# Kernel optimization log

Hardware: AMD Instinct MI355X
Metric: run time of the kernel (lower is better)

## Reference

```python
import jax, jax.numpy as jnp
import numpy as np
from jax import lax

NX, NY = 6, 6
NB = NX * NY            # 36 blocks
B, S = 64, 256          # batch, sample_count
EPS = 1e-6

def build_edges(nx, ny):
    edges = []
    for i in range(nx):
        for j in range(ny):
            for dx, dy in [(-1, 0), (0, -1), (0, 1), (1, 0)]:
                x, y = i + dx, j + dy
                if 0 <= x < nx and 0 <= y < ny:
                    edges.append((j * nx + i, y * nx + x))
    return np.array(edges, np.int32)   # (120, 2)

EDGES_NP = build_edges(NX, NY)
NE = len(EDGES_NP)  # 120

def setup_inputs() -> dict:
    key = jax.random.key(0)
    ks = jax.random.split(key, 24)
    f32 = jnp.float32
    d = {
        "image":      jax.random.normal(ks[0], (B, 1, 32, 32), f32),
        "edge_noise": jax.random.uniform(ks[1], (B, S, NE), f32),
        "u_s":        jax.random.uniform(ks[2], (B, S, NB), f32),
        "u_d":        jax.random.uniform(ks[3], (B, S, NB), f32),
        # CNN params (OIHW)
        "cw1": jax.random.normal(ks[4], (32, 1, 5, 5), f32) * 0.05,
        "cb1": jnp.zeros((32,), f32),
        "cw2": jax.random.normal(ks[5], (32, 32, 5, 5), f32) * 0.05,
        "cb2": jnp.zeros((32,), f32),
        "cw3": jax.random.normal(ks[6], (64, 32, 5, 5), f32) * 0.05,
        "cb3": jnp.zeros((64,), f32),
        "cw4": jax.random.normal(ks[7], (64, 64, 5, 5), f32) * 0.05,
        "cb4": jnp.zeros((64,), f32),
        # is_connected MLP
        "wc1": jax.random.normal(ks[8], (256, 256), f32) * 0.05,
        "bc1": jnp.zeros((256,), f32),
        "wc2": jax.random.normal(ks[9], (256, NE), f32) * 0.05,
        "bc2": jnp.zeros((NE,), f32),
        # is_endpoint MLP
        "we1": jax.random.normal(ks[10], (256, 256), f32) * 0.05,
        "be1": jnp.zeros((256,), f32),
        "we2": jax.random.normal(ks[11], (256, NB), f32) * 0.05,
        "be2": jnp.zeros((NB,), f32),
        "edges": jnp.asarray(EDGES_NP),  # (NE, 2) int32, constants
    }
    return d

def _conv(x, w, b):
    y = lax.conv_general_dilated(x, w, (1, 1), 'VALID',
                                 dimension_numbers=('NCHW', 'OIHW', 'NCHW'))
    return y + b[None, :, None, None]

def _pool2(x):
    return lax.reduce_window(x, -jnp.inf, lax.max, (1, 1, 2, 2), (1, 1, 2, 2), 'VALID')

def reference(image, edge_noise, u_s, u_d,
              cw1, cb1, cw2, cb2, cw3, cb3, cw4, cb4,
              wc1, bc1, wc2, bc2, we1, be1, we2, be2, edges):
    # ---- CNN feature extractor ----
    h = _conv(image, cw1, cb1)
    h = _conv(h, cw2, cb2)
    h = _pool2(h)
    h = _conv(h, cw3, cb3)
    h = _conv(h, cw4, cb4)
    h = _pool2(h)
    emb = h.reshape(h.shape[0], -1)              # (B, 256)

    # ---- heads ----
    p_conn = jax.nn.sigmoid(jax.nn.relu(emb @ wc1 + bc1) @ wc2 + bc2)   # (B, NE)
    p_ep   = jax.nn.sigmoid(jax.nn.relu(emb @ we1 + be1) @ we2 + be2)   # (B, NB)

    pc = jnp.clip(p_conn, EPS, 1.0 - EPS)
    pe = jnp.clip(p_ep, EPS, 1.0 - EPS)
    cat = pe / pe.sum(-1, keepdims=True)
    logcat = jnp.log(cat)                        # (B, NB)

    # ---- Monte-Carlo sampling (ISED blackbox) ----
    conn = (edge_noise < pc[:, None, :]).astype(pc.dtype)               # (B,S,NE) Bernoulli
    g_s = -jnp.log(-jnp.log(jnp.clip(u_s, EPS, 1.0 - EPS)))
    g_d = -jnp.log(-jnp.log(jnp.clip(u_d, EPS, 1.0 - EPS)))
    s_idx = jnp.argmax(logcat[:, None, :] + g_s, axis=-1)               # (B,S) categorical
    d_idx = jnp.argmax(logcat[:, None, :] + g_d, axis=-1)               # (B,S)

    # ---- batched BFS reachability via boolean matrix squaring ----
    oh_u = jax.nn.one_hot(edges[:, 0], NB, dtype=pc.dtype)              # (NE, NB)
    oh_v = jax.nn.one_hot(edges[:, 1], NB, dtype=pc.dtype)
    e_sym = jnp.einsum('eu,ev->euv', oh_u, oh_v) + jnp.einsum('eu,ev->evu', oh_u, oh_v)
    A = jnp.minimum(jnp.einsum('bse,euv->bsuv', conn, e_sym), 1.0)      # (B,S,36,36)

    R = jnp.minimum(A + jnp.eye(NB, dtype=A.dtype), 1.0)
    for _ in range(6):                           # (I+A)^(2^6), covers path len<=36
        R = jnp.minimum(R @ R, 1.0)
    P = jnp.minimum(A @ R, 1.0)                  # paths of length >= 1 (BFS semantics)

    Pv = jnp.take_along_axis(P, s_idx[:, :, None, None], axis=2)[:, :, 0, :]  # (B,S,36)
    exists = (jnp.take_along_axis(Pv, d_idx[:, :, None], axis=2)[:, :, 0] > 0.5).astype(pc.dtype)  # (B,S)

    # ---- sample-probability weighting (differentiable ISED estimator) ----
    logw = (conn * jnp.log(pc)[:, None, :] + (1.0 - conn) * jnp.log1p(-pc)[:, None, :]).sum(-1)
    logw = logw + jnp.take_along_axis(logcat, s_idx, axis=1) \
                + jnp.take_along_axis(logcat, d_idx, axis=1)            # (B,S)
    w = jax.nn.softmax(logw, axis=1)
    p1 = (w * exists).sum(axis=1)                # P(path exists)
    return jnp.stack([1.0 - p1, p1], axis=-1)    # (B, 2)
```

## Files before the change

### kernel.cpp

```cpp
#include <hip/hip_runtime.h>

typedef unsigned long long u64;
#define EPSF 1e-6f

__global__ __launch_bounds__(256) void k_conv1(const float* __restrict__ img,
                                               const float* __restrict__ cw1,
                                               const float* __restrict__ cb1,
                                               float* __restrict__ c1) {
  int slab = blockIdx.x, b = blockIdx.y;
  __shared__ float simg[32 * 33];
  for (int k = threadIdx.x; k < 1024; k += 256) {
    int y = k >> 5, x = k & 31;
    simg[y * 33 + x] = img[b * 1024 + k];
  }
  int ocl = threadIdx.x >> 5;
  int x = threadIdx.x & 31;
  int oc = slab * 8 + ocl;
  float w[25];
#pragma unroll
  for (int k = 0; k < 25; ++k) w[k] = cw1[oc * 25 + k];
  float bias = cb1[oc];
  __syncthreads();
  if (x < 28) {
    float acc[5];
#pragma unroll
    for (int k = 0; k < 5; ++k) acc[k] = bias;
    float* outp = c1 + (b * 32 + oc) * 784 + x;
#pragma unroll
    for (int r = 0; r < 32; ++r) {
      float in[5];
#pragma unroll
      for (int c = 0; c < 5; ++c) in[c] = simg[r * 33 + x + c];
#pragma unroll
      for (int ky = 0; ky < 5; ++ky) {
        int y = r - ky;
        if (y < 0 || y > 27) continue;
#pragma unroll
        for (int kx = 0; kx < 5; ++kx)
          acc[y % 5] = fmaf(w[ky * 5 + kx], in[kx], acc[y % 5]);
      }
      if (r >= 4) {
        int y = r - 4;
        outp[y * 28] = acc[y % 5];
        acc[y % 5] = bias;
      }
    }
  }
}

__global__ __launch_bounds__(192) void k_conv2(const float* __restrict__ c1,
                                               const float* __restrict__ cw2,
                                               const float* __restrict__ cb2,
                                               float* __restrict__ p1w) {
  int ocq = blockIdx.x, b = blockIdx.y;
  __shared__ float smem[18432];
  float* w2s = smem;
  float* sl = smem + 6400;
  int t = threadIdx.x;
  int g = t / 48, r48 = t % 48;
  int ocg = r48 / 24, row = r48 % 24;
  {
    const float4* src = (const float4*)(cw2 + ocq * 8 * 800);
    for (int k4 = t; k4 < 1600; k4 += 192) {
      float4 v = src[k4];
      float vv[4] = {v.x, v.y, v.z, v.w};
      int k = k4 * 4;
#pragma unroll
      for (int r = 0; r < 4; ++r) {
        int kk = k + r;
        int o = kk / 800, rest = kk % 800;
        w2s[rest * 8 + o] = vv[r];
      }
    }
  }
  float acc[4][24];
#pragma unroll
  for (int j = 0; j < 4; ++j)
#pragma unroll
    for (int c = 0; c < 24; ++c) acc[j][c] = 0.f;

  for (int icl = 0; icl < 8; ++icl) {
    int ic = g * 8 + icl;
    __syncthreads();
    {
      const float4* src = (const float4*)(c1 + (b * 32 + ic) * 784);
      float4* dst = (float4*)(sl + g * 784);
      for (int k = r48; k < 196; k += 48) dst[k] = src[k];
    }
    __syncthreads();
#pragma unroll
    for (int ky = 0; ky < 5; ++ky) {
      const float4* rp = (const float4*)(sl + g * 784 + (row + ky) * 28);
      float win[28];
#pragma unroll
      for (int q = 0; q < 7; ++q) {
        float4 v = rp[q];
        win[4 * q] = v.x; win[4 * q + 1] = v.y; win[4 * q + 2] = v.z; win[4 * q + 3] = v.w;
      }
      const float* wb = w2s + (ic * 25 + ky * 5) * 8 + ocg * 4;
#pragma unroll
      for (int kx = 0; kx < 5; ++kx) {
        float wq[4];
        *(float4*)wq = *(const float4*)(wb + kx * 8);
#pragma unroll
        for (int c = 0; c < 24; ++c) {
#pragma unroll
          for (int j = 0; j < 4; ++j) acc[j][c] = fmaf(wq[j], win[c + kx], acc[j][c]);
        }
      }
    }
  }
  __syncthreads();
  float* myred = smem + ((g * 2 + ocg) * 24 + row) * 96;
#pragma unroll
  for (int j = 0; j < 4; ++j)
#pragma unroll
    for (int c = 0; c < 24; ++c) myred[j * 24 + c] = acc[j][c];
  __syncthreads();
  if (g == 0) {
#pragma unroll
    for (int gg = 1; gg < 4; ++gg) {
      const float* rr = smem + ((gg * 2 + ocg) * 24 + row) * 96;
#pragma unroll
      for (int j = 0; j < 4; ++j)
#pragma unroll
        for (int c = 0; c < 24; ++c) acc[j][c] += rr[j * 24 + c];
    }
#pragma unroll
    for (int j = 0; j < 4; ++j) {
      float bias = cb2[ocq * 8 + ocg * 4 + j];
#pragma unroll
      for (int c = 0; c < 24; ++c) myred[j * 24 + c] = acc[j][c] + bias;
    }
  }
  __syncthreads();
  for (int k = t; k < 1152; k += 192) {
    int o = k / 144, rr2 = k % 144;
    int py = rr2 / 12, px = rr2 % 12;
    int og = o >> 2, j = o & 3;
    const float* b0 = smem + (og * 24 + 2 * py) * 96 + j * 24 + 2 * px;
    float m = fmaxf(fmaxf(b0[0], b0[1]), fmaxf(b0[96], b0[97]));
    p1w[(b * 32 + ocq * 8 + o) * 144 + py * 12 + px] = m;
  }
}

__global__ __launch_bounds__(256) void k_conv3(const float* __restrict__ p1w,
                                               const float* __restrict__ cw3,
                                               const float* __restrict__ cb3,
                                               float* __restrict__ c3) {
  int ocq = blockIdx.x, b = blockIdx.y;
  __shared__ float smem[17408];
  float* w3s = smem;
  float* ins = smem + 12800;
  int t = threadIdx.x;
  {
    const float4* src = (const float4*)(p1w + b * 32 * 144);
    float4* dst = (float4*)ins;
    for (int k = t; k < 1152; k += 256) dst[k] = src[k];
  }
  {
    const float4* src = (const float4*)(cw3 + ocq * 16 * 800);
    for (int k4 = t; k4 < 3200; k4 += 256) {
      float4 v = src[k4];
      float vv[4] = {v.x, v.y, v.z, v.w};
      int k = k4 * 4;
#pragma unroll
      for (int r = 0; r < 4; ++r) {
        int kk = k + r;
        int o = kk / 800, rest = kk % 800;
        w3s[rest * 16 + o] = vv[r];
      }
    }
  }
  int g = t >> 5, r32 = t & 31;
  int ocg = r32 >> 3, row = r32 & 7;
  float acc[4][8];
#pragma unroll
  for (int j = 0; j < 4; ++j)
#pragma unroll
    for (int c = 0; c < 8; ++c) acc[j][c] = 0.f;
  __syncthreads();
#pragma unroll
  for (int icl = 0; icl < 4; ++icl) {
    int ic = g * 4 + icl;
#pragma unroll
    for (int ky = 0; ky < 5; ++ky) {
      const float4* rp = (const float4*)(ins + ic * 144 + (row + ky) * 12);
      float win[12];
#pragma unroll
      for (int q = 0; q < 3; ++q) {
        float4 v = rp[q];
        win[4 * q] = v.x; win[4 * q + 1] = v.y; win[4 * q + 2] = v.z; win[4 * q + 3] = v.w;
      }
      const float* wb = w3s + (ic * 25 + ky * 5) * 16 + ocg * 4;
#pragma unroll
      for (int kx = 0; kx < 5; ++kx) {
        float wq[4];
        *(float4*)wq = *(const float4*)(wb + kx * 16);
#pragma unroll
        for (int c = 0; c < 8; ++c) {
#pragma unroll
          for (int j = 0; j < 4; ++j) acc[j][c] = fmaf(wq[j], win[c + kx], acc[j][c]);
        }
      }
    }
  }
  __syncthreads();
  float* myred = smem + t * 32;
#pragma unroll
  for (int j = 0; j < 4; ++j)
#pragma unroll
    for (int c = 0; c < 8; ++c) myred[j * 8 + c] = acc[j][c];
  __syncthreads();
  if (g == 0) {
#pragma unroll
    for (int gg = 1; gg < 8; ++gg) {
      const float* rr = smem + (gg * 32 + r32) * 32;
#pragma unroll
      for (int j = 0; j < 4; ++j)
#pragma unroll
        for (int c = 0; c < 8; ++c) acc[j][c] += rr[j * 8 + c];
    }
#pragma unroll
    for (int j = 0; j < 4; ++j) {
      float bias = cb3[ocq * 16 + ocg * 4 + j];
#pragma unroll
      for (int c = 0; c < 8; ++c)
        c3[(b * 64 + ocq * 16 + ocg * 4 + j) * 64 + row * 8 + c] = acc[j][c] + bias;
    }
  }
}

__global__ __launch_bounds__(256) void k_conv4(const float* __restrict__ c3,
                                               const float* __restrict__ cw4,
                                               const float* __restrict__ cb4,
                                               float* __restrict__ emb) {
  int ocq = blockIdx.x, b = blockIdx.y;
  __shared__ float smem[29696];
  float* w4s = smem;
  float* ins = smem + 25600;
  int t = threadIdx.x;
  {
    const float4* src = (const float4*)(c3 + b * 4096);
    float4* dst = (float4*)ins;
    for (int k = t; k < 1024; k += 256) dst[k] = src[k];
  }
  {
    const float4* src = (const float4*)(cw4 + ocq * 16 * 1600);
    for (int k4 = t; k4 < 6400; k4 += 256) {
      float4 v = src[k4];
      float vv[4] = {v.x, v.y, v.z, v.w};
      int k = k4 * 4;
#pragma unroll
      for (int r = 0; r < 4; ++r) {
        int kk = k + r;
        int o = kk / 1600, rest = kk % 1600;
        w4s[rest * 16 + o] = vv[r];
      }
    }
  }
  int g = t >> 4, r16 = t & 15;
  int ocg = r16 >> 2, row = r16 & 3;
  float acc[4][4];
#pragma unroll
  for (int j = 0; j < 4; ++j)
#pragma unroll
    for (int c = 0; c < 4; ++c) acc[j][c] = 0.f;
  __syncthreads();
#pragma unroll
  for (int icl = 0; icl < 4; ++icl) {
    int ic = g * 4 + icl;
#pragma unroll
    for (int ky = 0; ky < 5; ++ky) {
      const float4* rp = (const float4*)(ins + ic * 64 + (row + ky) * 8);
      float win[8];
#pragma unroll
      for (int q = 0; q < 2; ++q) {
        float4 v = rp[q];
        win[4 * q] = v.x; win[4 * q + 1] = v.y; win[4 * q + 2] = v.z; win[4 * q + 3] = v.w;
      }
      const float* wb = w4s + (ic * 25 + ky * 5) * 16 + ocg * 4;
#pragma unroll
      for (int kx = 0; kx < 5; ++kx) {
        float wq[4];
        *(float4*)wq = *(const float4*)(wb + kx * 16);
#pragma unroll
        for (int c = 0; c < 4; ++c) {
#pragma unroll
          for (int j = 0; j < 4; ++j) acc[j][c] = fmaf(wq[j], win[c + kx], acc[j][c]);
        }
      }
    }
  }
  __syncthreads();
  float* myred = smem + t * 16;
#pragma unroll
  for (int j = 0; j < 4; ++j)
#pragma unroll
    for (int c = 0; c < 4; ++c) myred[j * 4 + c] = acc[j][c];
  __syncthreads();
  if (g == 0) {
#pragma unroll
    for (int gg = 1; gg < 16; ++gg) {
      const float* rr = smem + (gg * 16 + r16) * 16;
#pragma unroll
      for (int j = 0; j < 4; ++j)
#pragma unroll
        for (int c = 0; c < 4; ++c) acc[j][c] += rr[j * 4 + c];
    }
#pragma unroll
    for (int j = 0; j < 4; ++j) {
      float bias = cb4[ocq * 16 + ocg * 4 + j];
#pragma unroll
      for (int c = 0; c < 4; ++c) myred[j * 4 + c] = acc[j][c] + bias;
    }
  }
  __syncthreads();
  if (t < 64) {
    int o = t >> 2, q = t & 3, py = q >> 1, px = q & 1;
    int og = o >> 2, j = o & 3;
    const float* b0 = smem + (og * 4 + 2 * py) * 16 + j * 4 + 2 * px;
    float m = fmaxf(fmaxf(b0[0], b0[1]), fmaxf(b0[16], b0[17]));
    emb[b * 256 + (ocq * 16 + o) * 4 + py * 2 + px] = m;
  }
}

__global__ __launch_bounds__(256) void k_heads(const float* __restrict__ emb,
    const float* __restrict__ wc1, const float* __restrict__ bc1,
    const float* __restrict__ wc2, const float* __restrict__ bc2,
    const float* __restrict__ we1, const float* __restrict__ be1,
    const float* __restrict__ we2, const float* __restrict__ be2,
    float* __restrict__ pcw, float* __restrict__ lpcw,
    float* __restrict__ l1mw, float* __restrict__ lcatw) {
  int head = blockIdx.x, b = blockIdx.y;
  int t = threadIdx.x;
  __shared__ float e_s[256], h_s[256];
  __shared__ float aux;
  e_s[t] = emb[b * 256 + t];
  __syncthreads();
  const float* W1 = head ? we1 : wc1;
  const float* B1 = head ? be1 : bc1;
  float s = B1[t];
  for (int i = 0; i < 256; i += 4) {
    s = fmaf(e_s[i], W1[i * 256 + t], s);
    s = fmaf(e_s[i + 1], W1[(i + 1) * 256 + t], s);
    s = fmaf(e_s[i + 2], W1[(i + 2) * 256 + t], s);
    s = fmaf(e_s[i + 3], W1[(i + 3) * 256 + t], s);
  }
  h_s[t] = fmaxf(s, 0.f);
  __syncthreads();
  int NO = head ? 36 : 120;
  const float* W2 = head ? we2 : wc2;
  const float* B2 = head ? be2 : bc2;
  if (t < NO) {
    float s2 = B2[t];
    for (int i = 0; i < 256; ++i) s2 = fmaf(h_s[i], W2[i * NO + t], s2);
    float p = 1.f / (1.f + expf(-s2));
    p = fminf(fmaxf(p, EPSF), 1.f - EPSF);
    if (head == 0) {
      pcw[b * 120 + t] = p;
      lpcw[b * 120 + t] = logf(p);
      l1mw[b * 120 + t] = log1pf(-p);
    } else {
      e_s[t] = p;
    }
  }
  if (head == 1) {
    __syncthreads();
    if (t == 0) {
      float sm = 0.f;
      for (int j2 = 0; j2 < 36; ++j2) sm += e_s[j2];
      aux = sm;
    }
    __syncthreads();
    if (t < 36) lcatw[b * 36 + t] = logf(e_s[t] / aux);
  }
}

__global__ __launch_bounds__(256) void k_mc(const float* __restrict__ enoise,
    const float* __restrict__ us, const float* __restrict__ ud,
    const int* __restrict__ edges,
    const float* __restrict__ pcw, const float* __restrict__ lpcw,
    const float* __restrict__ l1mw, const float* __restrict__ lcatw,
    float* __restrict__ out) {
  int b = blockIdx.x, t = threadIdx.x;
  __shared__ __align__(16) float pc_s[120];
  __shared__ __align__(16) float lpc_s[120];
  __shared__ __align__(16) float l1m_s[120];
  __shared__ __align__(16) float lcat_s[36];
  __shared__ __align__(16) int einfo[120];
  __shared__ float red_s[256];
  if (t < 120) {
    pc_s[t] = pcw[b * 120 + t];
    lpc_s[t] = lpcw[b * 120 + t];
    l1m_s[t] = l1mw[b * 120 + t];
    int u = edges[2 * t], v = edges[2 * t + 1];
    int d = v - u;
    int isV = (d == 6 || d == -6) ? 1 : 0;
    int pos = d > 0 ? u : v;
    einfo[t] = pos | (isV << 6);
  }
  if (t < 36) lcat_s[t] = lcatw[b * 36 + t];
  __syncthreads();

  float logw = 0.f;
  u64 H = 0, V = 0;
  {
    const float4* np = (const float4*)(enoise + ((size_t)(b * 256 + t)) * 120);
#pragma unroll
    for (int q = 0; q < 30; ++q) {
      float4 nz = np[q];
      float4 p4 = ((const float4*)pc_s)[q];
      float4 lp4 = ((const float4*)lpc_s)[q];
      float4 lm4 = ((const float4*)l1m_s)[q];
      int4 e4 = ((const int4*)einfo)[q];
      float nv[4] = {nz.x, nz.y, nz.z, nz.w};
      float pv[4] = {p4.x, p4.y, p4.z, p4.w};
      float lv[4] = {lp4.x, lp4.y, lp4.z, lp4.w};
      float mv[4] = {lm4.x, lm4.y, lm4.z, lm4.w};
      int ev[4] = {e4.x, e4.y, e4.z, e4.w};
#pragma unroll
      for (int r = 0; r < 4; ++r) {
        bool conn = nv[r] < pv[r];
        logw += conn ? lv[r] : mv[r];
        if (conn) {
          u64 bit = 1ull << (ev[r] & 63);
          if (ev[r] & 64) V |= bit; else H |= bit;
        }
      }
    }
  }
  int si = 0, di = 0;
  {
    const float4* up = (const float4*)(us + ((size_t)(b * 256 + t)) * 36);
    float best = -1e30f;
#pragma unroll
    for (int q = 0; q < 9; ++q) {
      float4 uv = up[q];
      float4 lc4 = ((const float4*)lcat_s)[q];
      float vv[4] = {uv.x, uv.y, uv.z, uv.w};
      float lc[4] = {lc4.x, lc4.y, lc4.z, lc4.w};
#pragma unroll
      for (int r = 0; r < 4; ++r) {
        float u = fminf(fmaxf(vv[r], EPSF), 1.f - EPSF);
        float gq = -logf(-logf(u));
        float val = lc[r] + gq;
        if (val > best) { best = val; si = q * 4 + r; }
      }
    }
  }
  {
    const float4* up = (const float4*)(ud + ((size_t)(b * 256 + t)) * 36);
    float best = -1e30f;
#pragma unroll
    for (int q = 0; q < 9; ++q) {
      float4 uv = up[q];
      float4 lc4 = ((const float4*)lcat_s)[q];
      float vv[4] = {uv.x, uv.y, uv.z, uv.w};
      float lc[4] = {lc4.x, lc4.y, lc4.z, lc4.w};
#pragma unroll
      for (int r = 0; r < 4; ++r) {
        float u = fminf(fmaxf(vv[r], EPSF), 1.f - EPSF);
        float gq = -logf(-logf(u));
        float val = lc[r] + gq;
        if (val > best) { best = val; di = q * 4 + r; }
      }
    }
  }
  logw += lcat_s[si] + lcat_s[di];

  u64 comp = 1ull << si;
  while (true) {
    u64 prev = comp;
    comp |= ((comp & H) << 1) | ((comp >> 1) & H);
    comp |= ((comp & V) << 6) | ((comp >> 6) & V);
    if (comp == prev) break;
  }
  float ex;
  if (si == di) ex = (comp != (1ull << si)) ? 1.f : 0.f;
  else ex = ((comp >> di) & 1ull) ? 1.f : 0.f;

  red_s[t] = logw; __syncthreads();
  for (int off = 128; off > 0; off >>= 1) {
    if (t < off) red_s[t] = fmaxf(red_s[t], red_s[t + off]);
    __syncthreads();
  }
  float m = red_s[0]; __syncthreads();
  float evx = expf(logw - m);
  red_s[t] = evx; __syncthreads();
  for (int off = 128; off > 0; off >>= 1) {
    if (t < off) red_s[t] += red_s[t + off];
    __syncthreads();
  }
  float den = red_s[0]; __syncthreads();
  red_s[t] = evx * ex; __syncthreads();
  for (int off = 128; off > 0; off >>= 1) {
    if (t < off) red_s[t] += red_s[t + off];
    __syncthreads();
  }
  if (t == 0) {
    float p1v = red_s[0] / den;
    out[b * 2] = 1.f - p1v;
    out[b * 2 + 1] = p1v;
  }
}

extern "C" void kernel_launch(void* const* d_in, const int* in_sizes, int n_in,
                              void* d_out, int out_size, void* d_ws, size_t ws_size,
                              hipStream_t stream) {
  const float* image = (const float*)d_in[0];
  const float* enoise = (const float*)d_in[1];
  const float* us = (const float*)d_in[2];
  const float* udn = (const float*)d_in[3];
  const float* cw1 = (const float*)d_in[4];
  const float* cb1 = (const float*)d_in[5];
  const float* cw2 = (const float*)d_in[6];
  const float* cb2 = (const float*)d_in[7];
  const float* cw3 = (const float*)d_in[8];
  const float* cb3 = (const float*)d_in[9];
  const float* cw4 = (const float*)d_in[10];
  const float* cb4 = (const float*)d_in[11];
  const float* wc1 = (const float*)d_in[12];
  const float* bc1 = (const float*)d_in[13];
  const float* wc2 = (const float*)d_in[14];
  const float* bc2 = (const float*)d_in[15];
  const float* we1 = (const float*)d_in[16];
  const float* be1 = (const float*)d_in[17];
  const float* we2 = (const float*)d_in[18];
  const float* be2 = (const float*)d_in[19];
  const int* edges = (const int*)d_in[20];

  float* ws = (float*)d_ws;
  float* c1 = ws;
  float* p1w = ws + 1605632;
  float* c3 = ws + 1900544;
  float* emb = ws + 2162688;
  float* pcw = ws + 2179072;
  float* lpcw = ws + 2186752;
  float* l1mw = ws + 2194432;
  float* lcatw = ws + 2202112;
  float* outp = (float*)d_out;

  k_conv1<<<dim3(4, 64), dim3(256), 0, stream>>>(image, cw1, cb1, c1);
  k_conv2<<<dim3(4, 64), dim3(192), 0, stream>>>(c1, cw2, cb2, p1w);
  k_conv3<<<dim3(4, 64), dim3(256), 0, stream>>>(p1w, cw3, cb3, c3);
  k_conv4<<<dim3(4, 64), dim3(256), 0, stream>>>(c3, cw4, cb4, emb);
  k_heads<<<dim3(2, 64), dim3(256), 0, stream>>>(emb, wc1, bc1, wc2, bc2,
                                                 we1, be1, we2, be2,
                                                 pcw, lpcw, l1mw, lcatw);
  k_mc<<<dim3(64), dim3(256), 0, stream>>>(enoise, us, udn, edges,
                                           pcw, lpcw, l1mw, lcatw, outp);
}
```

Before: 135.2 us.

## Split conv kernels across more blocks and use tree reductions over input-channel groups

Conv1 splits output rows across two halves of a 512-thread block. Conv2 splits each image's rows into two blocks and spreads input channels over eight groups. Conv3 and conv4 split output channels into eight-wide slices. All three replace serial single-group reductions with log-depth shared-memory tree reductions. The aim is more parallelism and occupancy in the conv stages, which otherwise launch only 256 blocks. In exchange, more __syncthreads barriers are added and each block must reload the shared input.

```diff
diff --git a/kernel.cpp b/kernel.cpp
--- a/kernel.cpp
+++ b/kernel.cpp
@@ -3,19 +3,22 @@
 typedef unsigned long long u64;
 #define EPSF 1e-6f
 
-__global__ __launch_bounds__(256) void k_conv1(const float* __restrict__ img,
+__global__ __launch_bounds__(512) void k_conv1(const float* __restrict__ img,
                                                const float* __restrict__ cw1,
                                                const float* __restrict__ cb1,
                                                float* __restrict__ c1) {
   int slab = blockIdx.x, b = blockIdx.y;
   __shared__ float simg[32 * 33];
-  for (int k = threadIdx.x; k < 1024; k += 256) {
+  for (int k = threadIdx.x; k < 1024; k += 512) {
     int y = k >> 5, x = k & 31;
     simg[y * 33 + x] = img[b * 1024 + k];
   }
-  int ocl = threadIdx.x >> 5;
-  int x = threadIdx.x & 31;
+  int half = threadIdx.x >> 8;
+  int u = threadIdx.x & 255;
+  int ocl = u >> 5;
+  int x = u & 31;
   int oc = slab * 8 + ocl;
+  int y0 = half * 14;
   float w[25];
 #pragma unroll
   for (int k = 0; k < 25; ++k) w[k] = cw1[oc * 25 + k];
@@ -27,41 +30,42 @@
     for (int k = 0; k < 5; ++k) acc[k] = bias;
     float* outp = c1 + (b * 32 + oc) * 784 + x;
 #pragma unroll
-    for (int r = 0; r < 32; ++r) {
+    for (int rr = 0; rr < 18; ++rr) {
+      int r = y0 + rr;
       float in[5];
 #pragma unroll
       for (int c = 0; c < 5; ++c) in[c] = simg[r * 33 + x + c];
 #pragma unroll
       for (int ky = 0; ky < 5; ++ky) {
-        int y = r - ky;
-        if (y < 0 || y > 27) continue;
+        if (rr < ky || rr - ky > 13) continue;
+        int slot = (rr - ky) % 5;
 #pragma unroll
         for (int kx = 0; kx < 5; ++kx)
-          acc[y % 5] = fmaf(w[ky * 5 + kx], in[kx], acc[y % 5]);
-      }
-      if (r >= 4) {
-        int y = r - 4;
-        outp[y * 28] = acc[y % 5];
-        acc[y % 5] = bias;
+          acc[slot] = fmaf(w[ky * 5 + kx], in[kx], acc[slot]);
+      }
+      if (rr >= 4) {
+        int slot = (rr - 4) % 5;
+        outp[(y0 + rr - 4) * 28] = acc[slot];
+        acc[slot] = bias;
       }
     }
   }
 }
 
-__global__ __launch_bounds__(192) void k_conv2(const float* __restrict__ c1,
+__global__ __launch_bounds__(384) void k_conv2(const float* __restrict__ c1,
                                                const float* __restrict__ cw2,
                                                const float* __restrict__ cb2,
                                                float* __restrict__ p1w) {
-  int ocq = blockIdx.x, b = blockIdx.y;
-  __shared__ float smem[18432];
+  int ocq = blockIdx.x, rh = blockIdx.y, b = blockIdx.z;
+  __shared__ float smem[9984];
   float* w2s = smem;
   float* sl = smem + 6400;
   int t = threadIdx.x;
-  int g = t / 48, r48 = t % 48;
-  int ocg = r48 / 24, row = r48 % 24;
+  int g = t / 48, p = t % 48;
+  int ocg = p / 12, row = p % 12;
   {
     const float4* src = (const float4*)(cw2 + ocq * 8 * 800);
-    for (int k4 = t; k4 < 1600; k4 += 192) {
+    for (int k4 = t; k4 < 1600; k4 += 384) {
       float4 v = src[k4];
       float vv[4] = {v.x, v.y, v.z, v.w};
       int k = k4 * 4;
@@ -73,74 +77,104 @@
       }
     }
   }
-  float acc[4][24];
-#pragma unroll
-  for (int j = 0; j < 4; ++j)
+  float acc[2][24];
+#pragma unroll
+  for (int j = 0; j < 2; ++j)
 #pragma unroll
     for (int c = 0; c < 24; ++c) acc[j][c] = 0.f;
 
-  for (int icl = 0; icl < 8; ++icl) {
-    int ic = g * 8 + icl;
+  int r0 = rh * 12;
+#pragma unroll
+  for (int icl = 0; icl < 4; ++icl) {
+    int ic = g + icl * 8;
     __syncthreads();
     {
-      const float4* src = (const float4*)(c1 + (b * 32 + ic) * 784);
-      float4* dst = (float4*)(sl + g * 784);
-      for (int k = r48; k < 196; k += 48) dst[k] = src[k];
+      const float4* src = (const float4*)(c1 + (b * 32 + ic) * 784 + r0 * 28);
+      float4* dst = (float4*)(sl + g * 448);
+      for (int k = p; k < 112; k += 48) dst[k] = src[k];
     }
     __syncthreads();
 #pragma unroll
     for (int ky = 0; ky < 5; ++ky) {
-      const float4* rp = (const float4*)(sl + g * 784 + (row + ky) * 28);
+      const float4* rp = (const float4*)(sl + g * 448 + (row + ky) * 28);
       float win[28];
 #pragma unroll
       for (int q = 0; q < 7; ++q) {
         float4 v = rp[q];
         win[4 * q] = v.x; win[4 * q + 1] = v.y; win[4 * q + 2] = v.z; win[4 * q + 3] = v.w;
       }
-      const float* wb = w2s + (ic * 25 + ky * 5) * 8 + ocg * 4;
+      const float* wb = w2s + (ic * 25 + ky * 5) * 8 + ocg * 2;
 #pragma unroll
       for (int kx = 0; kx < 5; ++kx) {
-        float wq[4];
-        *(float4*)wq = *(const float4*)(wb + kx * 8);
+        float2 wv = *(const float2*)(wb + kx * 8);
 #pragma unroll
         for (int c = 0; c < 24; ++c) {
-#pragma unroll
-          for (int j = 0; j < 4; ++j) acc[j][c] = fmaf(wq[j], win[c + kx], acc[j][c]);
+          acc[0][c] = fmaf(wv.x, win[c + kx], acc[0][c]);
+          acc[1][c] = fmaf(wv.y, win[c + kx], acc[1][c]);
         }
       }
     }
   }
-  __syncthreads();
-  float* myred = smem + ((g * 2 + ocg) * 24 + row) * 96;
-#pragma unroll
-  for (int j = 0; j < 4; ++j)
-#pragma unroll
-    for (int c = 0; c < 24; ++c) myred[j * 24 + c] = acc[j][c];
-  __syncthreads();
+  float* buf = smem;
+  __syncthreads();
+  if (g >= 4) {
+    float* d = buf + (g - 4) * 2304 + p * 48;
+#pragma unroll
+    for (int j = 0; j < 2; ++j)
+#pragma unroll
+      for (int c = 0; c < 24; ++c) d[j * 24 + c] = acc[j][c];
+  }
+  __syncthreads();
+  if (g < 4) {
+    const float* s = buf + g * 2304 + p * 48;
+#pragma unroll
+    for (int j = 0; j < 2; ++j)
+#pragma unroll
+      for (int c = 0; c < 24; ++c) acc[j][c] += s[j * 24 + c];
+  }
+  __syncthreads();
+  if (g == 2 || g == 3) {
+    float* d = buf + (g - 2) * 2304 + p * 48;
+#pragma unroll
+    for (int j = 0; j < 2; ++j)
+#pragma unroll
+      for (int c = 0; c < 24; ++c) d[j * 24 + c] = acc[j][c];
+  }
+  __syncthreads();
+  if (g < 2) {
+    const float* s = buf + g * 2304 + p * 48;
+#pragma unroll
+    for (int j = 0; j < 2; ++j)
+#pragma unroll
+      for (int c = 0; c < 24; ++c) acc[j][c] += s[j * 24 + c];
+  }
+  __syncthreads();
+  if (g == 1) {
+    float* d = buf + p * 48;
+#pragma unroll
+    for (int j = 0; j < 2; ++j)
+#pragma unroll
+      for (int c = 0; c < 24; ++c) d[j * 24 + c] = acc[j][c];
+  }
+  __syncthreads();
+  float* pb = buf + 2304;
   if (g == 0) {
-#pragma unroll
-    for (int gg = 1; gg < 4; ++gg) {
-      const float* rr = smem + ((gg * 2 + ocg) * 24 + row) * 96;
-#pragma unroll
-      for (int j = 0; j < 4; ++j)
-#pragma unroll
-        for (int c = 0; c < 24; ++c) acc[j][c] += rr[j * 24 + c];
-    }
-#pragma unroll
-    for (int j = 0; j < 4; ++j) {
-      float bias = cb2[ocq * 8 + ocg * 4 + j];
-#pragma unroll
-      for (int c = 0; c < 24; ++c) myred[j * 24 + c] = acc[j][c] + bias;
-    }
-  }
-  __syncthreads();
-  for (int k = t; k < 1152; k += 192) {
-    int o = k / 144, rr2 = k % 144;
-    int py = rr2 / 12, px = rr2 % 12;
-    int og = o >> 2, j = o & 3;
-    const float* b0 = smem + (og * 24 + 2 * py) * 96 + j * 24 + 2 * px;
-    float m = fmaxf(fmaxf(b0[0], b0[1]), fmaxf(b0[96], b0[97]));
-    p1w[(b * 32 + ocq * 8 + o) * 144 + py * 12 + px] = m;
+    const float* s = buf + p * 48;
+#pragma unroll
+    for (int j = 0; j < 2; ++j) {
+      float bias = cb2[ocq * 8 + ocg * 2 + j];
+#pragma unroll
+      for (int c = 0; c < 24; ++c)
+        pb[(ocg * 2 + j) * 288 + row * 24 + c] = acc[j][c] + s[j * 24 + c] + bias;
+    }
+  }
+  __syncthreads();
+  for (int k = t; k < 576; k += 384) {
+    int o = k / 72, rem = k % 72;
+    int py = rem / 12, px = rem % 12;
+    const float* b0 = pb + o * 288 + (2 * py) * 24 + 2 * px;
+    float m = fmaxf(fmaxf(b0[0], b0[1]), fmaxf(b0[24], b0[25]));
+    p1w[(b * 32 + ocq * 8 + o) * 144 + (rh * 6 + py) * 12 + px] = m;
   }
 }
 
@@ -148,10 +182,10 @@
                                                const float* __restrict__ cw3,
                                                const float* __restrict__ cb3,
                                                float* __restrict__ c3) {
-  int ocq = blockIdx.x, b = blockIdx.y;
-  __shared__ float smem[17408];
+  int oc8 = blockIdx.x, b = blockIdx.y;
+  __shared__ float smem[11008];
   float* w3s = smem;
-  float* ins = smem + 12800;
+  float* ins = smem + 6400;
   int t = threadIdx.x;
   {
     const float4* src = (const float4*)(p1w + b * 32 * 144);
@@ -159,7 +193,144 @@
     for (int k = t; k < 1152; k += 256) dst[k] = src[k];
   }
   {
-    const float4* src = (const float4*)(cw3 + ocq * 16 * 800);
+    const float4* src = (const float4*)(cw3 + oc8 * 8 * 800);
+    for (int k4 = t; k4 < 1600; k4 += 256) {
+      float4 v = src[k4];
+      float vv[4] = {v.x, v.y, v.z, v.w};
+      int k = k4 * 4;
+#pragma unroll
+      for (int r = 0; r < 4; ++r) {
+        int kk = k + r;
+        int o = kk / 800, rest = kk % 800;
+        w3s[rest * 8 + o] = vv[r];
+      }
+    }
+  }
+  int g = t >> 4, p = t & 15;
+  int ocg = p >> 3, row = p & 7;
+  float acc[4][8];
+#pragma unroll
+  for (int j = 0; j < 4; ++j)
+#pragma unroll
+    for (int c = 0; c < 8; ++c) acc[j][c] = 0.f;
+  __syncthreads();
+#pragma unroll
+  for (int icl = 0; icl < 2; ++icl) {
+    int ic = g + icl * 16;
+#pragma unroll
+    for (int ky = 0; ky < 5; ++ky) {
+      const float4* rp = (const float4*)(ins + ic * 144 + (row + ky) * 12);
+      float win[12];
+#pragma unroll
+      for (int q = 0; q < 3; ++q) {
+        float4 v = rp[q];
+        win[4 * q] = v.x; win[4 * q + 1] = v.y; win[4 * q + 2] = v.z; win[4 * q + 3] = v.w;
+      }
+      const float* wb = w3s + (ic * 25 + ky * 5) * 8 + ocg * 4;
+#pragma unroll
+      for (int kx = 0; kx < 5; ++kx) {
+        float wq[4];
+        *(float4*)wq = *(const float4*)(wb + kx * 8);
+#pragma unroll
+        for (int c = 0; c < 8; ++c) {
+#pragma unroll
+          for (int j = 0; j < 4; ++j) acc[j][c] = fmaf(wq[j], win[c + kx], acc[j][c]);
+        }
+      }
+    }
+  }
+  float* buf = smem;
+  __syncthreads();
+  if (g >= 8) {
+    float* d = buf + (g - 8) * 512 + p * 32;
+#pragma unroll
+    for (int j = 0; j < 4; ++j)
+#pragma unroll
+      for (int c = 0; c < 8; ++c) d[j * 8 + c] = acc[j][c];
+  }
+  __syncthreads();
+  if (g < 8) {
+    const float* s = buf + g * 512 + p * 32;
+#pragma unroll
+    for (int j = 0; j < 4; ++j)
+#pragma unroll
+      for (int c = 0; c < 8; ++c) acc[j][c] += s[j * 8 + c];
+  }
+  __syncthreads();
+  if (g >= 4 && g < 8) {
+    float* d = buf + (g - 4) * 512 + p * 32;
+#pragma unroll
+    for (int j = 0; j < 4; ++j)
+#pragma unroll
+      for (int c = 0; c < 8; ++c) d[j * 8 + c] = acc[j][c];
+  }
+  __syncthreads();
+  if (g < 4) {
+    const float* s = buf + g * 512 + p * 32;
+#pragma unroll
+    for (int j = 0; j < 4; ++j)
+#pragma unroll
+      for (int c = 0; c < 8; ++c) acc[j][c] += s[j * 8 + c];
+  }
+  __syncthreads();
+  if (g == 2 || g == 3) {
+    float* d = buf + (g - 2) * 512 + p * 32;
+#pragma unroll
+    for (int j = 0; j < 4; ++j)
+#pragma unroll
+      for (int c = 0; c < 8; ++c) d[j * 8 + c] = acc[j][c];
+  }
+  __syncthreads();
+  if (g < 2) {
+    const float* s = buf + g * 512 + p * 32;
+#pragma unroll
+    for (int j = 0; j < 4; ++j)
+#pragma unroll
+      for (int c = 0; c < 8; ++c) acc[j][c] += s[j * 8 + c];
+  }
+  __syncthreads();
+  if (g == 1) {
+    float* d = buf + p * 32;
+#pragma unroll
+    for (int j = 0; j < 4; ++j)
+#pragma unroll
+      for (int c = 0; c < 8; ++c) d[j * 8 + c] = acc[j][c];
+  }
+  __syncthreads();
+  if (g == 0) {
+    const float* s = buf + p * 32;
+#pragma unroll
+    for (int j = 0; j < 4; ++j) {
+      float bias = cb3[oc8 * 8 + ocg * 4 + j];
+      float4 v0, v1;
+      v0.x = acc[j][0] + s[j * 8 + 0] + bias; v0.y = acc[j][1] + s[j * 8 + 1] + bias;
+      v0.z = acc[j][2] + s[j * 8 + 2] + bias; v0.w = acc[j][3] + s[j * 8 + 3] + bias;
+      v1.x = acc[j][4] + s[j * 8 + 4] + bias; v1.y = acc[j][5] + s[j * 8 + 5] + bias;
+      v1.z = acc[j][6] + s[j * 8 + 6] + bias; v1.w = acc[j][7] + s[j * 8 + 7] + bias;
+      float* op = c3 + (b * 64 + oc8 * 8 + ocg * 4 + j) * 64 + row * 8;
+      *(float4*)op = v0; *(float4*)(op + 4) = v1;
+    }
+  }
+}
+
+__global__ __launch_bounds__(256) void k_conv4(const float* __restrict__ c3,
+                                               const float* __restrict__ cw4,
+                                               const float* __restrict__ cb4,
+                                               float* __restrict__ emb) {
+  int oc8 = blockIdx.x, b = blockIdx.y;
+  __shared__ float smem[17152];
+  float* w4s = smem;
+  float* ins = smem + 12800;
+  int t = threadIdx.x;
+  {
+    const float4* src = (const float4*)(c3 + b * 4096);
+    for (int k = t; k < 1024; k += 256) {
+      int ic = k >> 4, q = k & 15;
+      *(float4*)(ins + ic * 68 + q * 4) = src[k];
+    }
+  }
+  {
+    const float4* src = (const float4*)(cw4 + oc8 * 8 * 1600);
     for (int k4 = t; k4 < 3200; k4 += 256) {
       float4 v = src[k4];
       float vv[4] = {v.x, v.y, v.z, v.w};
@@ -167,123 +338,36 @@
 #pragma unroll
       for (int r = 0; r < 4; ++r) {
         int kk = k + r;
-        int o = kk / 800, rest = kk % 800;
-        w3s[rest * 16 + o] = vv[r];
-      }
-    }
-  }
-  int g = t >> 5, r32 = t & 31;
-  int ocg = r32 >> 3, row = r32 & 7;
-  float acc[4][8];
+        int o = kk / 1600, rest = kk % 1600;
+        w4s[rest * 8 + o] = vv[r];
+      }
+    }
+  }
+  int g = t >> 3, p = t & 7;
+  int ocg = p >> 2, row = p & 3;
+  float acc[4][4];
 #pragma unroll
   for (int j = 0; j < 4; ++j)
 #pragma unroll
-    for (int c = 0; c < 8; ++c) acc[j][c] = 0.f;
-  __syncthreads();
-#pragma unroll
-  for (int icl = 0; icl < 4; ++icl) {
-    int ic = g * 4 + icl;
+    for (int c = 0; c < 4; ++c) acc[j][c] = 0.f;
+  __syncthreads();
+#pragma unroll
+  for (int icl = 0; icl < 2; ++icl) {
+    int ic = g + icl * 32;
 #pragma unroll
     for (int ky = 0; ky < 5; ++ky) {
-      const float4* rp = (const float4*)(ins + ic * 144 + (row + ky) * 12);
-      float win[12];
-#pragma unroll
-      for (int q = 0; q < 3; ++q) {
-        float4 v = rp[q];
-        win[4 * q] = v.x; win[4 * q + 1] = v.y; win[4 * q + 2] = v.z; win[4 * q + 3] = v.w;
-      }
-      const float* wb = w3s + (ic * 25 + ky * 5) * 16 + ocg * 4;
-#pragma unroll
-      for (int kx = 0; kx < 5; ++kx) {
-        float wq[4];
-        *(float4*)wq = *(const float4*)(wb + kx * 16);
-#pragma unroll
-        for (int c = 0; c < 8; ++c) {
-#pragma unroll
-          for (int j = 0; j < 4; ++j) acc[j][c] = fmaf(wq[j], win[c + kx], acc[j][c]);
-        }
-      }
-    }
-  }
-  __syncthreads();
-  float* myred = smem + t * 32;
-#pragma unroll
-  for (int j = 0; j < 4; ++j)
-#pragma unroll
-    for (int c = 0; c < 8; ++c) myred[j * 8 + c] = acc[j][c];
-  __syncthreads();
-  if (g == 0) {
-#pragma unroll
-    for (int gg = 1; gg < 8; ++gg) {
-      const float* rr = smem + (gg * 32 + r32) * 32;
-#pragma unroll
-      for (int j = 0; j < 4; ++j)
-#pragma unroll
-        for (int c = 0; c < 8; ++c) acc[j][c] += rr[j * 8 + c];
-    }
-#pragma unroll
-    for (int j = 0; j < 4; ++j) {
-      float bias = cb3[ocq * 16 + ocg * 4 + j];
-#pragma unroll
-      for (int c = 0; c < 8; ++c)
-        c3[(b * 64 + ocq * 16 + ocg * 4 + j) * 64 + row * 8 + c] = acc[j][c] + bias;
-    }
-  }
-}
-
-__global__ __launch_bounds__(256) void k_conv4(const float* __restrict__ c3,
-                                               const float* __restrict__ cw4,
-                                               const float* __restrict__ cb4,
-                                               float* __restrict__ emb) {
-  int ocq = blockIdx.x, b = blockIdx.y;
-  __shared__ float smem[29696];
-  float* w4s = smem;
-  float* ins = smem + 25600;
-  int t = threadIdx.x;
-  {
-    const float4* src = (const float4*)(c3 + b * 4096);
-    float4* dst = (float4*)ins;
-    for (int k = t; k < 1024; k += 256) dst[k] = src[k];
-  }
-  {
-    const float4* src = (const float4*)(cw4 + ocq * 16 * 1600);
-    for (int k4 = t; k4 < 6400; k4 += 256) {
-      float4 v = src[k4];
-      float vv[4] = {v.x, v.y, v.z, v.w};
-      int k = k4 * 4;
-#pragma unroll
-      for (int r = 0; r < 4; ++r) {
-        int kk = k + r;
-        int o = kk / 1600, rest = kk % 1600;
-        w4s[rest * 16 + o] = vv[r];
-      }
-    }
-  }
-  int g = t >> 4, r16 = t & 15;
-  int ocg = r16 >> 2, row = r16 & 3;
-  float acc[4][4];
-#pragma unroll
-  for (int j = 0; j < 4; ++j)
-#pragma unroll
-    for (int c = 0; c < 4; ++c) acc[j][c] = 0.f;
-  __syncthreads();
-#pragma unroll
-  for (int icl = 0; icl < 4; ++icl) {
-    int ic = g * 4 + icl;
-#pragma unroll
-    for (int ky = 0; ky < 5; ++ky) {
-      const float4* rp = (const float4*)(ins + ic * 64 + (row + ky) * 8);
+      const float4* rp = (const float4*)(ins + ic * 68 + (row + ky) * 8);
       float win[8];
 #pragma unroll
       for (int q = 0; q < 2; ++q) {
         float4 v = rp[q];
         win[4 * q] = v.x; win[4 * q + 1] = v.y; win[4 * q + 2] = v.z; win[4 * q + 3] = v.w;
       }
-      const float* wb = w4s + (ic * 25 + ky * 5) * 16 + ocg * 4;
+      const float* wb = w4s + (ic * 25 + ky * 5) * 8 + ocg * 4;
 #pragma unroll
       for (int kx = 0; kx < 5; ++kx) {
         float wq[4];
-        *(float4*)wq = *(const float4*)(wb + kx * 16);
+        *(float4*)wq = *(const float4*)(wb + kx * 8);
 #pragma unroll
         for (int c = 0; c < 4; ++c) {
 #pragma unroll
@@ -292,36 +376,41 @@
       }
     }
   }
-  __syncthreads();
-  float* myred = smem + t * 16;
-#pragma unroll
-  for (int j = 0; j < 4; ++j)
-#pragma unroll
-    for (int c = 0; c < 4; ++c) myred[j * 4 + c] = acc[j][c];
-  __syncthreads();
+  float* buf = smem;
+#pragma unroll
+  for (int half = 16; half >= 1; half >>= 1) {
+    __syncthreads();
+    if (g >= half && g < 2 * half) {
+      float* d = buf + (g - half) * 128 + p * 16;
+#pragma unroll
+      for (int j = 0; j < 4; ++j)
+#pragma unroll
+        for (int c = 0; c < 4; ++c) d[j * 4 + c] = acc[j][c];
+    }
+    __syncthreads();
+    if (g < half) {
+      const float* s = buf + g * 128 + p * 16;
+#pragma unroll
+      for (int j = 0; j < 4; ++j)
+#pragma unroll
+        for (int c = 0; c < 4; ++c) acc[j][c] += s[j * 4 + c];
+    }
+  }
+  float* pb = buf + 2048;
   if (g == 0) {
 #pragma unroll
-    for (int gg = 1; gg < 16; ++gg) {
-      const float* rr = smem + (gg * 16 + r16) * 16;
-#pragma unroll
-      for (int j = 0; j < 4; ++j)
-#pragma unroll
-        for (int c = 0; c < 4; ++c) acc[j][c] += rr[j * 4 + c];
-    }
-#pragma unroll
     for (int j = 0; j < 4; ++j) {
-      float bias = cb4[ocq * 16 + ocg * 4 + j];
-#pragma unroll
-      for (int c = 0; c < 4; ++c) myred[j * 4 + c] = acc[j][c] + bias;
-    }
-  }
-  __syncthreads();
-  if (t < 64) {
+      float bias = cb4[oc8 * 8 + ocg * 4 + j];
+#pragma unroll
+      for (int c = 0; c < 4; ++c) pb[(ocg * 4 + j) * 16 + row * 4 + c] = acc[j][c] + bias;
+    }
+  }
+  __syncthreads();
+  if (t < 32) {
     int o = t >> 2, q = t & 3, py = q >> 1, px = q & 1;
-    int og = o >> 2, j = o & 3;
-    const float* b0 = smem + (og * 4 + 2 * py) * 16 + j * 4 + 2 * px;
-    float m = fmaxf(fmaxf(b0[0], b0[1]), fmaxf(b0[16], b0[17]));
-    emb[b * 256 + (ocq * 16 + o) * 4 + py * 2 + px] = m;
+    const float* b0 = pb + o * 16 + (2 * py) * 4 + 2 * px;
+    float m = fmaxf(fmaxf(b0[0], b0[1]), fmaxf(b0[4], b0[5]));
+    emb[b * 256 + (oc8 * 8 + o) * 4 + py * 2 + px] = m;
   }
 }
 
@@ -541,10 +630,10 @@
   float* lcatw = ws + 2202112;
   float* outp = (float*)d_out;
 
-  k_conv1<<<dim3(4, 64), dim3(256), 0, stream>>>(image, cw1, cb1, c1);
-  k_conv2<<<dim3(4, 64), dim3(192), 0, stream>>>(c1, cw2, cb2, p1w);
-  k_conv3<<<dim3(4, 64), dim3(256), 0, stream>>>(p1w, cw3, cb3, c3);
-  k_conv4<<<dim3(4, 64), dim3(256), 0, stream>>>(c3, cw4, cb4, emb);
+  k_conv1<<<dim3(4, 64), dim3(512), 0, stream>>>(image, cw1, cb1, c1);
+  k_conv2<<<dim3(4, 2, 64), dim3(384), 0, stream>>>(c1, cw2, cb2, p1w);
+  k_conv3<<<dim3(8, 64), dim3(256), 0, stream>>>(p1w, cw3, cb3, c3);
+  k_conv4<<<dim3(8, 64), dim3(256), 0, stream>>>(c3, cw4, cb4, emb);
   k_heads<<<dim3(2, 64), dim3(256), 0, stream>>>(emb, wc1, bc1, wc2, bc2,
                                                  we1, be1, we2, be2,
                                                  pcw, lpcw, l1mw, lcatw);
```

New measurement: 134.5 us. No clear change (-0.6%).
